# Optimization experiments

Measured on AMD Instinct MI355X. Metric: run time of the kernel, lower is better.

Reference implementation:

```python
import jax, jax.numpy as jnp
import numpy as np

N, D, I, O = 4096, 64, 512, 512  # samples, node_nums (bases), input_size, output_size


def setup_inputs() -> dict:
    key = jax.random.key(0)
    k1, k2, k3, k4 = jax.random.split(key, 4)
    # xavier_uniform bounds
    w_bound = float(np.sqrt(6.0 / (I + O)))
    b_bound = float(np.sqrt(6.0 / (D + O)))
    return {
        "x": jax.random.normal(k1, (N, I), dtype=jnp.float32),
        "var_vector": jax.random.uniform(k2, (N, D), dtype=jnp.float32),
        "W_1": jax.random.uniform(k3, (D, I, O), dtype=jnp.float32, minval=-w_bound, maxval=w_bound),
        "b_1": jax.random.uniform(k4, (D, O), dtype=jnp.float32, minval=-b_bound, maxval=b_bound),
    }


def reference(x, var_vector, W_1, b_1):
    # Math identical to: einsum('nd,dio->nio') then bmm(x[:,None,:], W)[:,0,:] + b.
    # Reordered contraction: contract x against each basis first (never forms n,i,o).
    y = jnp.einsum('ni,dio->ndo', x, W_1)        # [n, d, o]
    out = jnp.einsum('nd,ndo->no', var_vector, y)  # [n, o]
    b = jnp.einsum('nd,do->no', var_vector, b_1)   # [n, o]
    return out + b
```

## Files before the change

### kernel.cpp

```cpp
#include <hip/hip_runtime.h>
#include <hip/hip_bf16.h>
#include <stdint.h>
#include <stddef.h>

#define N_ 4096
#define D_ 64
#define I_ 512
#define O_ 512

#define BM 256
#define BN 128
#define SPLITS 4
#define DPG 16
#define PAIRS (DPG / 2)
#define KXS 16
#define NS (PAIRS * KXS)
#define SLOTA (128 * 128)
#define SLOTB (64 * 128)

typedef float  floatx4 __attribute__((ext_vector_type(4)));
typedef short  shortx8 __attribute__((ext_vector_type(8)));
typedef __bf16 bf16x8  __attribute__((ext_vector_type(8)));

__device__ __forceinline__ void gload_lds16(const void* g, void* l) {
  __builtin_amdgcn_global_load_lds(
      (const __attribute__((address_space(1))) void*)g,
      (__attribute__((address_space(3))) void*)l, 16, 0, 0);
}

__device__ __forceinline__ unsigned short f2bf(float f) {
  union { float f; unsigned int u; } c; c.f = f;
  unsigned int u = c.u;
  return (unsigned short)((u + 0x7fffu + ((u >> 16) & 1u)) >> 16);
}

__device__ __forceinline__ void mfma_bf16(floatx4& c, shortx8 a, shortx8 b) {
  union { shortx8 s; bf16x8 h; } ua, ub;
  ua.s = a; ub.s = b;
  c = __builtin_amdgcn_mfma_f32_16x16x32_bf16(ua.h, ub.h, c, 0, 0, 0);
}

__global__ void k_cvt_x(const float* __restrict__ x, unsigned short* __restrict__ xb) {
  int idx = (blockIdx.x * blockDim.x + threadIdx.x) * 8;
  floatx4 a = *(const floatx4*)(x + idx);
  floatx4 b = *(const floatx4*)(x + idx + 4);
  shortx8 o;
  o[0] = (short)f2bf(a[0]); o[1] = (short)f2bf(a[1]);
  o[2] = (short)f2bf(a[2]); o[3] = (short)f2bf(a[3]);
  o[4] = (short)f2bf(b[0]); o[5] = (short)f2bf(b[1]);
  o[6] = (short)f2bf(b[2]); o[7] = (short)f2bf(b[3]);
  *(shortx8*)(xb + idx) = o;
}

__global__ void k_cvt_w(const float* __restrict__ w, unsigned short* __restrict__ wt) {
  __shared__ unsigned short T[64][72];
  int bid = blockIdx.x;
  int d  = bid >> 6;
  int it = (bid >> 3) & 7;
  int ot = bid & 7;
  int i0 = it * 64, o0 = ot * 64;
  int t = threadIdx.x;
  const float* wp = w + ((size_t)d * I_ + i0) * O_ + o0;
  #pragma unroll
  for (int j = 0; j < 16; ++j) {
    int idx = j * 256 + t;
    int r = idx >> 6, c = idx & 63;
    T[r][c] = f2bf(wp[(size_t)r * O_ + c]);
  }
  __syncthreads();
  unsigned short* op = wt + ((size_t)d * O_ + o0) * I_ + i0;
  #pragma unroll
  for (int j = 0; j < 16; ++j) {
    int idx = j * 256 + t;
    int r = idx >> 6, c = idx & 63;
    op[(size_t)r * I_ + c] = T[c][r];
  }
}

__global__ void k_bias(const float* __restrict__ var, const float* __restrict__ b1,
                       float* __restrict__ out) {
  __shared__ float vs[16][64];
  int n0 = blockIdx.x * 16;
  int t = threadIdx.x;
  #pragma unroll
  for (int j = 0; j < 4; ++j) {
    int idx = j * 256 + t;
    vs[idx >> 6][idx & 63] = var[(size_t)n0 * D_ + idx];
  }
  __syncthreads();
  float a0[16], a1[16];
  #pragma unroll
  for (int r = 0; r < 16; ++r) { a0[r] = 0.f; a1[r] = 0.f; }
  for (int d = 0; d < D_; ++d) {
    float b0 = b1[(size_t)d * O_ + t];
    float bb = b1[(size_t)d * O_ + 256 + t];
    #pragma unroll
    for (int r = 0; r < 16; ++r) { a0[r] += vs[r][d] * b0; a1[r] += vs[r][d] * bb; }
  }
  #pragma unroll
  for (int r = 0; r < 16; ++r) {
    out[(size_t)(n0 + r) * O_ + t]       = a0[r];
    out[(size_t)(n0 + r) * O_ + 256 + t] = a1[r];
  }
}

__global__ __launch_bounds__(512) void k_gemm(
    const unsigned short* __restrict__ xb, const unsigned short* __restrict__ wt,
    const float* __restrict__ var, float* __restrict__ out) {
  __shared__ alignas(16) char lA[4][SLOTA];
  __shared__ alignas(16) char lB[4][2][SLOTB];
  __shared__ alignas(16) float lV[DPG * BM];

  const int tid = threadIdx.x;
  const int bid = blockIdx.x;
  const int g  = bid & 15;
  const int mt = bid >> 4;
  const int ot = g >> 2, split = g & 3;
  const int brow = mt * BM, bcol = ot * BN, d0 = split * DPG;

  const int lane = tid & 63, wid = tid >> 6;
  const int wr = wid >> 1, wc = wid & 1;
  const int l15 = lane & 15, l4 = lane >> 4;

  #pragma unroll
  for (int j = 0; j < (DPG * BM) / 512; ++j) {
    int idx = j * 512 + tid;
    int dd = idx >> 8, row = idx & (BM - 1);
    lV[idx] = var[(size_t)(brow + row) * D_ + d0 + dd];
  }

  const char* xbB = (const char*)xb;
  const char* wtB = (const char*)wt;

  int pbA[2]; size_t gbA[2];
  #pragma unroll
  for (int c = 0; c < 2; ++c) {
    int pb = (c * 512 + tid) << 4;
    int rl = pb >> 7;
    int colG = (pb & 127) ^ ((rl & 7) << 4);
    int r_src = rl + ((colG >> 6) << 7);
    int k_src = (colG & 63) >> 1;
    pbA[c] = pb;
    gbA[c] = ((size_t)(brow + r_src) * I_ + k_src) * 2;
  }
  int pbB; size_t gbB;
  {
    int pb = tid << 4;
    int rl = pb >> 7;
    int colG = (pb & 127) ^ ((rl & 7) << 4);
    int r_src = rl + ((colG >> 6) << 6);
    int k_src = (colG & 63) >> 1;
    pbB = pb;
    gbB = ((size_t)(bcol + r_src) * I_ + k_src) * 2;
  }

  int avOff[4], bvOff[4];
  #pragma unroll
  for (int m = 0; m < 4; ++m) {
    int r = wr * 64 + m * 16 + l15;
    int rl = r & 127;
    avOff[m] = rl * 128 + ((((r >> 7) << 6) + l4 * 16) ^ ((rl & 7) << 4));
  }
  #pragma unroll
  for (int n = 0; n < 4; ++n) {
    int r = wc * 64 + n * 16 + l15;
    int rl = r & 63;
    bvOff[n] = rl * 128 + (((wc << 6) + l4 * 16) ^ ((rl & 7) << 4));
  }

  auto stage_A = [&](int s) {
    const int kx = s & 15;
    char* la = (char*)&lA[s & 3][0];
    #pragma unroll
    for (int c = 0; c < 2; ++c)
      gload_lds16(xbB + gbA[c] + (size_t)kx * 64, la + pbA[c]);
  };
  auto stage_B = [&](int s) {
    const int d = d0 + 2 * (s >> 4);
    const int kx = s & 15;
    const char* src = wtB + (size_t)d * (I_ * O_ * 2) + gbB + (size_t)kx * 64;
    gload_lds16(src, (char*)&lB[s & 3][0][0] + pbB);
    gload_lds16(src + (size_t)(I_ * O_ * 2), (char*)&lB[s & 3][1][0] + pbB);
  };

  stage_A(0); stage_B(0); stage_A(1); stage_B(1);

  const floatx4 vzero = {0.f, 0.f, 0.f, 0.f};
  floatx4 master[4][4];
  #pragma unroll
  for (int m = 0; m < 4; ++m)
    #pragma unroll
    for (int n = 0; n < 4; ++n) master[m][n] = vzero;

  asm volatile("s_waitcnt vmcnt(4) lgkmcnt(0)" ::: "memory");
  __builtin_amdgcn_sched_barrier(0);
  __builtin_amdgcn_s_barrier();

  for (int p = 0; p < PAIRS; ++p) {
    floatx4 acc0[4][4], acc1[4][4];
    #pragma unroll
    for (int m = 0; m < 4; ++m)
      #pragma unroll
      for (int n = 0; n < 4; ++n) { acc0[m][n] = vzero; acc1[m][n] = vzero; }

    #pragma unroll 1
    for (int kx = 0; kx < KXS; ++kx) {
      const int s = p * KXS + kx;
      const char* aS  = (const char*)&lA[s & 3][0];
      const char* bS0 = (const char*)&lB[s & 3][0][0];
      const char* bS1 = (const char*)&lB[s & 3][1][0];
      shortx8 av[4], bv[4];

      #pragma unroll
      for (int m = 0; m < 4; ++m) av[m] = *(const shortx8*)(aS + avOff[m]);
      #pragma unroll
      for (int n = 0; n < 4; ++n) bv[n] = *(const shortx8*)(bS0 + bvOff[n]);
      if (s + 2 < NS) stage_A(s + 2);
      __builtin_amdgcn_s_barrier();
      asm volatile("s_waitcnt lgkmcnt(0)" ::: "memory");
      __builtin_amdgcn_sched_barrier(0);
      __builtin_amdgcn_s_setprio(1);
      #pragma unroll
      for (int m = 0; m < 4; ++m)
        #pragma unroll
        for (int n = 0; n < 4; ++n) mfma_bf16(acc0[m][n], av[m], bv[n]);
      __builtin_amdgcn_s_setprio(0);
      __builtin_amdgcn_s_barrier();

      #pragma unroll
      for (int n = 0; n < 4; ++n) bv[n] = *(const shortx8*)(bS1 + bvOff[n]);
      if (s + 2 < NS) stage_B(s + 2);
      __builtin_amdgcn_s_barrier();
      asm volatile("s_waitcnt lgkmcnt(0)" ::: "memory");
      __builtin_amdgcn_sched_barrier(0);
      __builtin_amdgcn_s_setprio(1);
      #pragma unroll
      for (int m = 0; m < 4; ++m)
        #pragma unroll
        for (int n = 0; n < 4; ++n) mfma_bf16(acc1[m][n], av[m], bv[n]);
      __builtin_amdgcn_s_setprio(0);
      if (s + 2 < NS) { asm volatile("s_waitcnt vmcnt(4)" ::: "memory"); }
      else            { asm volatile("s_waitcnt vmcnt(0)" ::: "memory"); }
      __builtin_amdgcn_s_barrier();
    }

    #pragma unroll
    for (int m = 0; m < 4; ++m) {
      int rbase = wr * 64 + m * 16 + l4 * 4;
      floatx4 v0 = *(const floatx4*)&lV[(2 * p) * BM + rbase];
      floatx4 v1 = *(const floatx4*)&lV[(2 * p + 1) * BM + rbase];
      #pragma unroll
      for (int n = 0; n < 4; ++n)
        #pragma unroll
        for (int r = 0; r < 4; ++r)
          master[m][n][r] += v0[r] * acc0[m][n][r] + v1[r] * acc1[m][n][r];
    }
  }

  #pragma unroll
  for (int m = 0; m < 4; ++m) {
    int row0 = brow + wr * 64 + m * 16 + l4 * 4;
    #pragma unroll
    for (int n = 0; n < 4; ++n) {
      int col = bcol + wc * 64 + n * 16 + l15;
      #pragma unroll
      for (int r = 0; r < 4; ++r)
        atomicAdd(out + (size_t)(row0 + r) * O_ + col, master[m][n][r]);
    }
  }
}

__global__ void k_naive(const float* __restrict__ x, const float* __restrict__ var,
                        const float* __restrict__ w, const float* __restrict__ b1,
                        float* __restrict__ out) {
  int n = blockIdx.x;
  int o = blockIdx.y * 128 + threadIdx.x;
  const float* xp = x + (size_t)n * I_;
  float acc = 0.f;
  for (int d = 0; d < D_; ++d) {
    const float* wp = w + (size_t)d * I_ * O_ + o;
    float y = 0.f;
    for (int i = 0; i < I_; ++i) y += xp[i] * wp[(size_t)i * O_];
    acc += var[(size_t)n * D_ + d] * (y + b1[(size_t)d * O_ + o]);
  }
  out[(size_t)n * O_ + o] = acc;
}

extern "C" void kernel_launch(void* const* d_in, const int* in_sizes, int n_in,
                              void* d_out, int out_size, void* d_ws, size_t ws_size,
                              hipStream_t stream) {
  const float* x   = (const float*)d_in[0];
  const float* var = (const float*)d_in[1];
  const float* W   = (const float*)d_in[2];
  const float* b1  = (const float*)d_in[3];
  float* out = (float*)d_out;

  const size_t wt_bytes = (size_t)D_ * I_ * O_ * 2;
  const size_t xb_bytes = (size_t)N_ * I_ * 2;
  if (ws_size >= wt_bytes + xb_bytes) {
    unsigned short* wt = (unsigned short*)d_ws;
    unsigned short* xb = (unsigned short*)((char*)d_ws + wt_bytes);
    k_cvt_x<<<dim3((N_ * I_) / (256 * 8)), dim3(256), 0, stream>>>(x, xb);
    k_cvt_w<<<dim3(D_ * 64), dim3(256), 0, stream>>>(W, wt);
    k_bias<<<dim3(N_ / 16), dim3(256), 0, stream>>>(var, b1, out);
    k_gemm<<<dim3((N_ / BM) * (O_ / BN) * SPLITS), dim3(512), 0, stream>>>(xb, wt, var, out);
  } else {
    k_naive<<<dim3(N_, O_ / 128), dim3(128), 0, stream>>>(x, var, W, b1, out);
  }
}
```

Measured before the change: 186.4 us.

## Shrink GEMM tile to 128x128 with 256 threads and simple double buffering

```diff
diff --git a/kernel.cpp b/kernel.cpp
--- a/kernel.cpp
+++ b/kernel.cpp
@@ -8,15 +8,14 @@
 #define I_ 512
 #define O_ 512
 
-#define BM 256
+#define BM 128
 #define BN 128
 #define SPLITS 4
 #define DPG 16
 #define PAIRS (DPG / 2)
 #define KXS 16
 #define NS (PAIRS * KXS)
-#define SLOTA (128 * 128)
-#define SLOTB (64 * 128)
+#define SLOT 8192
 
 typedef float  floatx4 __attribute__((ext_vector_type(4)));
 typedef short  shortx8 __attribute__((ext_vector_type(8)));
@@ -104,11 +103,11 @@
   }
 }
 
-__global__ __launch_bounds__(512) void k_gemm(
+__global__ __launch_bounds__(256, 2) void k_gemm(
     const unsigned short* __restrict__ xb, const unsigned short* __restrict__ wt,
     const float* __restrict__ var, float* __restrict__ out) {
-  __shared__ alignas(16) char lA[4][SLOTA];
-  __shared__ alignas(16) char lB[4][2][SLOTB];
+  __shared__ alignas(16) char lA[2][SLOT];
+  __shared__ alignas(16) char lB[2][2][SLOT];
   __shared__ alignas(16) float lV[DPG * BM];
 
   const int tid = threadIdx.x;
@@ -123,25 +122,25 @@
   const int l15 = lane & 15, l4 = lane >> 4;
 
   #pragma unroll
-  for (int j = 0; j < (DPG * BM) / 512; ++j) {
-    int idx = j * 512 + tid;
-    int dd = idx >> 8, row = idx & (BM - 1);
+  for (int j = 0; j < (DPG * BM) / 256; ++j) {
+    int idx = j * 256 + tid;
+    int dd = idx >> 7, row = idx & (BM - 1);
     lV[idx] = var[(size_t)(brow + row) * D_ + d0 + dd];
   }
 
   const char* xbB = (const char*)xb;
   const char* wtB = (const char*)wt;
-
-  int pbA[2]; size_t gbA[2];
-  #pragma unroll
-  for (int c = 0; c < 2; ++c) {
-    int pb = (c * 512 + tid) << 4;
+  const size_t IO2 = (size_t)I_ * O_ * 2;
+
+  int pbA; size_t gbA;
+  {
+    int pb = tid << 4;
     int rl = pb >> 7;
     int colG = (pb & 127) ^ ((rl & 7) << 4);
-    int r_src = rl + ((colG >> 6) << 7);
+    int r_src = rl + ((colG >> 6) << 6);
     int k_src = (colG & 63) >> 1;
-    pbA[c] = pb;
-    gbA[c] = ((size_t)(brow + r_src) * I_ + k_src) * 2;
+    pbA = pb;
+    gbA = ((size_t)(brow + r_src) * I_ + k_src) * 2;
   }
   int pbB; size_t gbB;
   {
@@ -157,104 +156,82 @@
   int avOff[4], bvOff[4];
   #pragma unroll
   for (int m = 0; m < 4; ++m) {
-    int r = wr * 64 + m * 16 + l15;
-    int rl = r & 127;
-    avOff[m] = rl * 128 + ((((r >> 7) << 6) + l4 * 16) ^ ((rl & 7) << 4));
-  }
-  #pragma unroll
-  for (int n = 0; n < 4; ++n) {
-    int r = wc * 64 + n * 16 + l15;
-    int rl = r & 63;
-    bvOff[n] = rl * 128 + (((wc << 6) + l4 * 16) ^ ((rl & 7) << 4));
-  }
-
-  auto stage_A = [&](int s) {
+    int rl = m * 16 + l15;
+    avOff[m] = rl * 128 + (((wr << 6) + l4 * 16) ^ ((rl & 7) << 4));
+    bvOff[m] = rl * 128 + (((wc << 6) + l4 * 16) ^ ((rl & 7) << 4));
+  }
+
+  auto stage = [&](int s, int buf) {
     const int kx = s & 15;
-    char* la = (char*)&lA[s & 3][0];
-    #pragma unroll
-    for (int c = 0; c < 2; ++c)
-      gload_lds16(xbB + gbA[c] + (size_t)kx * 64, la + pbA[c]);
+    const int d  = d0 + 2 * (s >> 4);
+    char* la  = (char*)&lA[buf][0];
+    char* lb0 = (char*)&lB[buf][0][0];
+    char* lb1 = (char*)&lB[buf][1][0];
+    const char* xsrc = xbB + gbA + (size_t)kx * 64;
+    const char* wsrc = wtB + (size_t)d * IO2 + gbB + (size_t)kx * 64;
+    #pragma unroll
+    for (int c = 0; c < 2; ++c) {
+      gload_lds16(xsrc + (size_t)c * 32768, la  + pbA + c * 4096);
+      gload_lds16(wsrc + (size_t)c * 32768, lb0 + pbB + c * 4096);
+      gload_lds16(wsrc + IO2 + (size_t)c * 32768, lb1 + pbB + c * 4096);
+    }
   };
-  auto stage_B = [&](int s) {
-    const int d = d0 + 2 * (s >> 4);
-    const int kx = s & 15;
-    const char* src = wtB + (size_t)d * (I_ * O_ * 2) + gbB + (size_t)kx * 64;
-    gload_lds16(src, (char*)&lB[s & 3][0][0] + pbB);
-    gload_lds16(src + (size_t)(I_ * O_ * 2), (char*)&lB[s & 3][1][0] + pbB);
-  };
-
-  stage_A(0); stage_B(0); stage_A(1); stage_B(1);
 
   const floatx4 vzero = {0.f, 0.f, 0.f, 0.f};
-  floatx4 master[4][4];
+  floatx4 master[4][4], acc0[4][4], acc1[4][4];
   #pragma unroll
   for (int m = 0; m < 4; ++m)
     #pragma unroll
-    for (int n = 0; n < 4; ++n) master[m][n] = vzero;
-
-  asm volatile("s_waitcnt vmcnt(4) lgkmcnt(0)" ::: "memory");
-  __builtin_amdgcn_sched_barrier(0);
-  __builtin_amdgcn_s_barrier();
-
-  for (int p = 0; p < PAIRS; ++p) {
-    floatx4 acc0[4][4], acc1[4][4];
+    for (int n = 0; n < 4; ++n) {
+      master[m][n] = vzero; acc0[m][n] = vzero; acc1[m][n] = vzero;
+    }
+
+  stage(0, 0);
+  __syncthreads();
+
+  #pragma unroll 1
+  for (int s = 0; s < NS; ++s) {
+    const int buf = s & 1;
+    if (s + 1 < NS) stage(s + 1, buf ^ 1);
+
+    const char* aS  = (const char*)&lA[buf][0];
+    const char* bS0 = (const char*)&lB[buf][0][0];
+    const char* bS1 = (const char*)&lB[buf][1][0];
+    shortx8 av[4], bv[4];
+    #pragma unroll
+    for (int m = 0; m < 4; ++m) av[m] = *(const shortx8*)(aS + avOff[m]);
+    #pragma unroll
+    for (int n = 0; n < 4; ++n) bv[n] = *(const shortx8*)(bS0 + bvOff[n]);
     #pragma unroll
     for (int m = 0; m < 4; ++m)
       #pragma unroll
-      for (int n = 0; n < 4; ++n) { acc0[m][n] = vzero; acc1[m][n] = vzero; }
-
-    #pragma unroll 1
-    for (int kx = 0; kx < KXS; ++kx) {
-      const int s = p * KXS + kx;
-      const char* aS  = (const char*)&lA[s & 3][0];
-      const char* bS0 = (const char*)&lB[s & 3][0][0];
-      const char* bS1 = (const char*)&lB[s & 3][1][0];
-      shortx8 av[4], bv[4];
-
-      #pragma unroll
-      for (int m = 0; m < 4; ++m) av[m] = *(const shortx8*)(aS + avOff[m]);
-      #pragma unroll
-      for (int n = 0; n < 4; ++n) bv[n] = *(const shortx8*)(bS0 + bvOff[n]);
-      if (s + 2 < NS) stage_A(s + 2);
-      __builtin_amdgcn_s_barrier();
-      asm volatile("s_waitcnt lgkmcnt(0)" ::: "memory");
-      __builtin_amdgcn_sched_barrier(0);
-      __builtin_amdgcn_s_setprio(1);
-      #pragma unroll
-      for (int m = 0; m < 4; ++m)
+      for (int n = 0; n < 4; ++n) mfma_bf16(acc0[m][n], av[m], bv[n]);
+    #pragma unroll
+    for (int n = 0; n < 4; ++n) bv[n] = *(const shortx8*)(bS1 + bvOff[n]);
+    #pragma unroll
+    for (int m = 0; m < 4; ++m)
+      #pragma unroll
+      for (int n = 0; n < 4; ++n) mfma_bf16(acc1[m][n], av[m], bv[n]);
+
+    if ((s & 15) == 15) {
+      int pp = s >> 4;
+      #pragma unroll
+      for (int m = 0; m < 4; ++m) {
+        int rbase = wr * 64 + m * 16 + l4 * 4;
+        floatx4 v0 = *(const floatx4*)&lV[(2 * pp) * BM + rbase];
+        floatx4 v1 = *(const floatx4*)&lV[(2 * pp + 1) * BM + rbase];
         #pragma unroll
-        for (int n = 0; n < 4; ++n) mfma_bf16(acc0[m][n], av[m], bv[n]);
-      __builtin_amdgcn_s_setprio(0);
-      __builtin_amdgcn_s_barrier();
-
-      #pragma unroll
-      for (int n = 0; n < 4; ++n) bv[n] = *(const shortx8*)(bS1 + bvOff[n]);
-      if (s + 2 < NS) stage_B(s + 2);
-      __builtin_amdgcn_s_barrier();
-      asm volatile("s_waitcnt lgkmcnt(0)" ::: "memory");
-      __builtin_amdgcn_sched_barrier(0);
-      __builtin_amdgcn_s_setprio(1);
-      #pragma unroll
-      for (int m = 0; m < 4; ++m)
-        #pragma unroll
-        for (int n = 0; n < 4; ++n) mfma_bf16(acc1[m][n], av[m], bv[n]);
-      __builtin_amdgcn_s_setprio(0);
-      if (s + 2 < NS) { asm volatile("s_waitcnt vmcnt(4)" ::: "memory"); }
-      else            { asm volatile("s_waitcnt vmcnt(0)" ::: "memory"); }
-      __builtin_amdgcn_s_barrier();
-    }
-
-    #pragma unroll
-    for (int m = 0; m < 4; ++m) {
-      int rbase = wr * 64 + m * 16 + l4 * 4;
-      floatx4 v0 = *(const floatx4*)&lV[(2 * p) * BM + rbase];
-      floatx4 v1 = *(const floatx4*)&lV[(2 * p + 1) * BM + rbase];
-      #pragma unroll
-      for (int n = 0; n < 4; ++n)
-        #pragma unroll
-        for (int r = 0; r < 4; ++r)
-          master[m][n][r] += v0[r] * acc0[m][n][r] + v1[r] * acc1[m][n][r];
-    }
+        for (int n = 0; n < 4; ++n) {
+          #pragma unroll
+          for (int r = 0; r < 4; ++r) {
+            master[m][n][r] += v0[r] * acc0[m][n][r] + v1[r] * acc1[m][n][r];
+            acc0[m][n][r] = 0.f;
+            acc1[m][n][r] = 0.f;
+          }
+        }
+      }
+    }
+    __syncthreads();
   }
 
   #pragma unroll
@@ -303,7 +280,7 @@
     k_cvt_x<<<dim3((N_ * I_) / (256 * 8)), dim3(256), 0, stream>>>(x, xb);
     k_cvt_w<<<dim3(D_ * 64), dim3(256), 0, stream>>>(W, wt);
     k_bias<<<dim3(N_ / 16), dim3(256), 0, stream>>>(var, b1, out);
-    k_gemm<<<dim3((N_ / BM) * (O_ / BN) * SPLITS), dim3(512), 0, stream>>>(xb, wt, var, out);
+    k_gemm<<<dim3((N_ / BM) * (O_ / BN) * SPLITS), dim3(256), 0, stream>>>(xb, wt, var, out);
   } else {
     k_naive<<<dim3(N_, O_ / 128), dim3(128), 0, stream>>>(x, var, W, b1, out);
   }
```

After: 199.0 us. 1.07x slower.

## Fold var scaling into A fragments and use a single accumulator with 256x256 tiles

Applied to the files above, without the earlier changes.

```diff
diff --git a/kernel.cpp b/kernel.cpp
--- a/kernel.cpp
+++ b/kernel.cpp
@@ -9,14 +9,10 @@
 #define O_ 512
 
 #define BM 256
-#define BN 128
-#define SPLITS 4
-#define DPG 16
-#define PAIRS (DPG / 2)
-#define KXS 16
-#define NS (PAIRS * KXS)
-#define SLOTA (128 * 128)
-#define SLOTB (64 * 128)
+#define BN 256
+#define SPLITS 8
+#define DPG 8
+#define NT 64
 
 typedef float  floatx4 __attribute__((ext_vector_type(4)));
 typedef short  shortx8 __attribute__((ext_vector_type(8)));
@@ -38,6 +34,20 @@
   union { shortx8 s; bf16x8 h; } ua, ub;
   ua.s = a; ub.s = b;
   c = __builtin_amdgcn_mfma_f32_16x16x32_bf16(ua.h, ub.h, c, 0, 0, 0);
+}
+
+__device__ __forceinline__ shortx8 scale_frag(shortx8 a, float v) {
+  union { shortx8 s; unsigned int u[4]; } x, r;
+  x.s = a;
+  #pragma unroll
+  for (int i = 0; i < 4; ++i) {
+    float lo = __uint_as_float(x.u[i] << 16) * v;
+    float hi = __uint_as_float(x.u[i] & 0xffff0000u) * v;
+    unsigned int ro;
+    asm("v_cvt_pk_bf16_f32 %0, %1, %2" : "=v"(ro) : "v"(lo), "v"(hi));
+    r.u[i] = ro;
+  }
+  return r.s;
 }
 
 __global__ void k_cvt_x(const float* __restrict__ x, unsigned short* __restrict__ xb) {
@@ -107,165 +117,191 @@
 __global__ __launch_bounds__(512) void k_gemm(
     const unsigned short* __restrict__ xb, const unsigned short* __restrict__ wt,
     const float* __restrict__ var, float* __restrict__ out) {
-  __shared__ alignas(16) char lA[4][SLOTA];
-  __shared__ alignas(16) char lB[4][2][SLOTB];
+  __shared__ alignas(16) char lA[2][2][16384];
+  __shared__ alignas(16) char lB[2][2][16384];
   __shared__ alignas(16) float lV[DPG * BM];
 
   const int tid = threadIdx.x;
   const int bid = blockIdx.x;
   const int g  = bid & 15;
   const int mt = bid >> 4;
-  const int ot = g >> 2, split = g & 3;
+  const int ot = g >> 3, split = g & 7;
   const int brow = mt * BM, bcol = ot * BN, d0 = split * DPG;
 
   const int lane = tid & 63, wid = tid >> 6;
-  const int wr = wid >> 1, wc = wid & 1;
+  const int wr = wid >> 2, wc = wid & 3;
   const int l15 = lane & 15, l4 = lane >> 4;
 
   #pragma unroll
   for (int j = 0; j < (DPG * BM) / 512; ++j) {
     int idx = j * 512 + tid;
-    int dd = idx >> 8, row = idx & (BM - 1);
-    lV[idx] = var[(size_t)(brow + row) * D_ + d0 + dd];
+    lV[idx] = var[(size_t)(brow + (idx & 255)) * D_ + d0 + (idx >> 8)];
   }
 
   const char* xbB = (const char*)xb;
   const char* wtB = (const char*)wt;
-
-  int pbA[2]; size_t gbA[2];
+  const size_t IO2 = (size_t)I_ * O_ * 2;
+
+  int pb[2]; size_t gA[2], gB[2];
   #pragma unroll
   for (int c = 0; c < 2; ++c) {
-    int pb = (c * 512 + tid) << 4;
-    int rl = pb >> 7;
-    int colG = (pb & 127) ^ ((rl & 7) << 4);
-    int r_src = rl + ((colG >> 6) << 7);
-    int k_src = (colG & 63) >> 1;
-    pbA[c] = pb;
-    gbA[c] = ((size_t)(brow + r_src) * I_ + k_src) * 2;
-  }
-  int pbB; size_t gbB;
-  {
-    int pb = tid << 4;
-    int rl = pb >> 7;
-    int colG = (pb & 127) ^ ((rl & 7) << 4);
-    int r_src = rl + ((colG >> 6) << 6);
-    int k_src = (colG & 63) >> 1;
-    pbB = pb;
-    gbB = ((size_t)(bcol + r_src) * I_ + k_src) * 2;
-  }
-
-  int avOff[4], bvOff[4];
-  #pragma unroll
-  for (int m = 0; m < 4; ++m) {
-    int r = wr * 64 + m * 16 + l15;
+    int p = (c * 512 + tid) << 4;
+    int rl = p >> 7;
+    int colG = (p & 127) ^ ((rl & 7) << 4);
+    int rs = rl + ((colG >> 6) << 7);
+    int ks = (colG & 63) >> 1;
+    pb[c] = p;
+    gA[c] = ((size_t)(brow + rs) * I_ + ks) * 2;
+    gB[c] = ((size_t)(bcol + rs) * I_ + ks) * 2;
+  }
+
+  int avOff[8], bvOff[4];
+  #pragma unroll
+  for (int m = 0; m < 8; ++m) {
+    int r = wr * 128 + m * 16 + l15;
     int rl = r & 127;
     avOff[m] = rl * 128 + ((((r >> 7) << 6) + l4 * 16) ^ ((rl & 7) << 4));
   }
   #pragma unroll
   for (int n = 0; n < 4; ++n) {
-    int r = wc * 64 + n * 16 + l15;
-    int rl = r & 63;
-    bvOff[n] = rl * 128 + (((wc << 6) + l4 * 16) ^ ((rl & 7) << 4));
-  }
-
-  auto stage_A = [&](int s) {
-    const int kx = s & 15;
-    char* la = (char*)&lA[s & 3][0];
-    #pragma unroll
-    for (int c = 0; c < 2; ++c)
-      gload_lds16(xbB + gbA[c] + (size_t)kx * 64, la + pbA[c]);
+    int c = wc * 64 + n * 16 + l15;
+    int rl = c & 127;
+    bvOff[n] = rl * 128 + ((((c >> 7) << 6) + l4 * 16) ^ ((rl & 7) << 4));
+  }
+
+  auto stgA = [&](int t, int kh) {
+    char* dst = &lA[t & 1][kh][0];
+    size_t ko = (size_t)((t & 7) * 128 + kh * 64);
+    gload_lds16(xbB + gA[0] + ko, dst + pb[0]);
+    gload_lds16(xbB + gA[1] + ko, dst + pb[1]);
   };
-  auto stage_B = [&](int s) {
-    const int d = d0 + 2 * (s >> 4);
-    const int kx = s & 15;
-    const char* src = wtB + (size_t)d * (I_ * O_ * 2) + gbB + (size_t)kx * 64;
-    gload_lds16(src, (char*)&lB[s & 3][0][0] + pbB);
-    gload_lds16(src + (size_t)(I_ * O_ * 2), (char*)&lB[s & 3][1][0] + pbB);
+  auto stgB = [&](int t, int kh) {
+    char* dst = &lB[t & 1][kh][0];
+    const char* src = wtB + (size_t)(d0 + (t >> 3)) * IO2
+                          + (size_t)((t & 7) * 128 + kh * 64);
+    gload_lds16(src + gB[0], dst + pb[0]);
+    gload_lds16(src + gB[1], dst + pb[1]);
   };
 
-  stage_A(0); stage_B(0); stage_A(1); stage_B(1);
-
   const floatx4 vzero = {0.f, 0.f, 0.f, 0.f};
-  floatx4 master[4][4];
-  #pragma unroll
-  for (int m = 0; m < 4; ++m)
-    #pragma unroll
-    for (int n = 0; n < 4; ++n) master[m][n] = vzero;
-
+  floatx4 acc[8][4];
+  #pragma unroll
+  for (int m = 0; m < 8; ++m)
+    #pragma unroll
+    for (int n = 0; n < 4; ++n) acc[m][n] = vzero;
+  float vv[8];
+
+  stgA(0, 0); stgB(0, 0); stgA(0, 1); stgB(0, 1);
   asm volatile("s_waitcnt vmcnt(4) lgkmcnt(0)" ::: "memory");
   __builtin_amdgcn_sched_barrier(0);
   __builtin_amdgcn_s_barrier();
-
-  for (int p = 0; p < PAIRS; ++p) {
-    floatx4 acc0[4][4], acc1[4][4];
+  __builtin_amdgcn_sched_barrier(0);
+
+  #pragma unroll 1
+  for (int t = 0; t < NT; ++t) {
+    const int buf = t & 1;
+    const char* a0 = &lA[buf][0][0];
+    const char* a1 = &lA[buf][1][0];
+    const char* b0 = &lB[buf][0][0];
+    const char* b1 = &lB[buf][1][0];
+    const bool pre = (t + 1 < NT);
+    shortx8 av[4], bv[4];
+
+    if ((t & 7) == 0) {
+      #pragma unroll
+      for (int m = 0; m < 8; ++m)
+        vv[m] = lV[((t >> 3) << 8) + wr * 128 + m * 16 + l15];
+    }
+
+    #pragma unroll
+    for (int m = 0; m < 4; ++m) av[m] = *(const shortx8*)(a0 + avOff[m]);
+    #pragma unroll
+    for (int n = 0; n < 4; ++n) bv[n] = *(const shortx8*)(b0 + bvOff[n]);
+    if (pre) stgA(t + 1, 0);
+    #pragma unroll
+    for (int m = 0; m < 4; ++m) av[m] = scale_frag(av[m], vv[m]);
+    __builtin_amdgcn_sched_barrier(0);
+    __builtin_amdgcn_s_barrier();
+    __builtin_amdgcn_sched_barrier(0);
+    __builtin_amdgcn_s_setprio(1);
     #pragma unroll
     for (int m = 0; m < 4; ++m)
       #pragma unroll
-      for (int n = 0; n < 4; ++n) { acc0[m][n] = vzero; acc1[m][n] = vzero; }
-
-    #pragma unroll 1
-    for (int kx = 0; kx < KXS; ++kx) {
-      const int s = p * KXS + kx;
-      const char* aS  = (const char*)&lA[s & 3][0];
-      const char* bS0 = (const char*)&lB[s & 3][0][0];
-      const char* bS1 = (const char*)&lB[s & 3][1][0];
-      shortx8 av[4], bv[4];
-
-      #pragma unroll
-      for (int m = 0; m < 4; ++m) av[m] = *(const shortx8*)(aS + avOff[m]);
-      #pragma unroll
-      for (int n = 0; n < 4; ++n) bv[n] = *(const shortx8*)(bS0 + bvOff[n]);
-      if (s + 2 < NS) stage_A(s + 2);
-      __builtin_amdgcn_s_barrier();
-      asm volatile("s_waitcnt lgkmcnt(0)" ::: "memory");
-      __builtin_amdgcn_sched_barrier(0);
-      __builtin_amdgcn_s_setprio(1);
-      #pragma unroll
-      for (int m = 0; m < 4; ++m)
-        #pragma unroll
-        for (int n = 0; n < 4; ++n) mfma_bf16(acc0[m][n], av[m], bv[n]);
-      __builtin_amdgcn_s_setprio(0);
-      __builtin_amdgcn_s_barrier();
-
-      #pragma unroll
-      for (int n = 0; n < 4; ++n) bv[n] = *(const shortx8*)(bS1 + bvOff[n]);
-      if (s + 2 < NS) stage_B(s + 2);
-      __builtin_amdgcn_s_barrier();
-      asm volatile("s_waitcnt lgkmcnt(0)" ::: "memory");
-      __builtin_amdgcn_sched_barrier(0);
-      __builtin_amdgcn_s_setprio(1);
-      #pragma unroll
-      for (int m = 0; m < 4; ++m)
-        #pragma unroll
-        for (int n = 0; n < 4; ++n) mfma_bf16(acc1[m][n], av[m], bv[n]);
-      __builtin_amdgcn_s_setprio(0);
-      if (s + 2 < NS) { asm volatile("s_waitcnt vmcnt(4)" ::: "memory"); }
-      else            { asm volatile("s_waitcnt vmcnt(0)" ::: "memory"); }
-      __builtin_amdgcn_s_barrier();
-    }
-
-    #pragma unroll
-    for (int m = 0; m < 4; ++m) {
-      int rbase = wr * 64 + m * 16 + l4 * 4;
-      floatx4 v0 = *(const floatx4*)&lV[(2 * p) * BM + rbase];
-      floatx4 v1 = *(const floatx4*)&lV[(2 * p + 1) * BM + rbase];
-      #pragma unroll
-      for (int n = 0; n < 4; ++n)
-        #pragma unroll
-        for (int r = 0; r < 4; ++r)
-          master[m][n][r] += v0[r] * acc0[m][n][r] + v1[r] * acc1[m][n][r];
-    }
-  }
-
-  #pragma unroll
-  for (int m = 0; m < 4; ++m) {
-    int row0 = brow + wr * 64 + m * 16 + l4 * 4;
+      for (int n = 0; n < 4; ++n) mfma_bf16(acc[m][n], av[m], bv[n]);
+    __builtin_amdgcn_s_setprio(0);
+    __builtin_amdgcn_sched_barrier(0);
+    __builtin_amdgcn_s_barrier();
+    __builtin_amdgcn_sched_barrier(0);
+
+    #pragma unroll
+    for (int m = 0; m < 4; ++m) av[m] = *(const shortx8*)(a0 + avOff[4 + m]);
+    if (pre) stgB(t + 1, 0);
+    #pragma unroll
+    for (int m = 0; m < 4; ++m) av[m] = scale_frag(av[m], vv[4 + m]);
+    __builtin_amdgcn_sched_barrier(0);
+    __builtin_amdgcn_s_barrier();
+    __builtin_amdgcn_sched_barrier(0);
+    __builtin_amdgcn_s_setprio(1);
+    #pragma unroll
+    for (int m = 0; m < 4; ++m)
+      #pragma unroll
+      for (int n = 0; n < 4; ++n) mfma_bf16(acc[4 + m][n], av[m], bv[n]);
+    __builtin_amdgcn_s_setprio(0);
+    if (pre) { asm volatile("s_waitcnt vmcnt(4)" ::: "memory"); }
+    else     { asm volatile("s_waitcnt vmcnt(0)" ::: "memory"); }
+    __builtin_amdgcn_sched_barrier(0);
+    __builtin_amdgcn_s_barrier();
+    __builtin_amdgcn_sched_barrier(0);
+
+    #pragma unroll
+    for (int m = 0; m < 4; ++m) av[m] = *(const shortx8*)(a1 + avOff[m]);
+    #pragma unroll
+    for (int n = 0; n < 4; ++n) bv[n] = *(const shortx8*)(b1 + bvOff[n]);
+    if (pre) stgA(t + 1, 1);
+    #pragma unroll
+    for (int m = 0; m < 4; ++m) av[m] = scale_frag(av[m], vv[m]);
+    __builtin_amdgcn_sched_barrier(0);
+    __builtin_amdgcn_s_barrier();
+    __builtin_amdgcn_sched_barrier(0);
+    __builtin_amdgcn_s_setprio(1);
+    #pragma unroll
+    for (int m = 0; m < 4; ++m)
+      #pragma unroll
+      for (int n = 0; n < 4; ++n) mfma_bf16(acc[m][n], av[m], bv[n]);
+    __builtin_amdgcn_s_setprio(0);
+    __builtin_amdgcn_sched_barrier(0);
+    __builtin_amdgcn_s_barrier();
+    __builtin_amdgcn_sched_barrier(0);
+
+    #pragma unroll
+    for (int m = 0; m < 4; ++m) av[m] = *(const shortx8*)(a1 + avOff[4 + m]);
+    if (pre) stgB(t + 1, 1);
+    #pragma unroll
+    for (int m = 0; m < 4; ++m) av[m] = scale_frag(av[m], vv[4 + m]);
+    __builtin_amdgcn_sched_barrier(0);
+    __builtin_amdgcn_s_barrier();
+    __builtin_amdgcn_sched_barrier(0);
+    __builtin_amdgcn_s_setprio(1);
+    #pragma unroll
+    for (int m = 0; m < 4; ++m)
+      #pragma unroll
+      for (int n = 0; n < 4; ++n) mfma_bf16(acc[4 + m][n], av[m], bv[n]);
+    __builtin_amdgcn_s_setprio(0);
+    if (pre) { asm volatile("s_waitcnt vmcnt(4)" ::: "memory"); }
+    __builtin_amdgcn_sched_barrier(0);
+    __builtin_amdgcn_s_barrier();
+    __builtin_amdgcn_sched_barrier(0);
+  }
+
+  #pragma unroll
+  for (int m = 0; m < 8; ++m) {
+    int row0 = brow + wr * 128 + m * 16 + l4 * 4;
     #pragma unroll
     for (int n = 0; n < 4; ++n) {
       int col = bcol + wc * 64 + n * 16 + l15;
       #pragma unroll
       for (int r = 0; r < 4; ++r)
-        atomicAdd(out + (size_t)(row0 + r) * O_ + col, master[m][n][r]);
+        atomicAdd(out + (size_t)(row0 + r) * O_ + col, acc[m][n][r]);
     }
   }
 }
```

Measured after the change: 258.1 us. +38.4%, slower.
